# Kernel tuning notes

Hardware: AMD Instinct MI355X
Metric: run time of the kernel (lower is better)

Reference implementation:

```python
import math
import jax, jax.numpy as jnp
import numpy as np

B, S, D = 8, 1024, 1024
H, DK = 16, 64
NUM_BUCKETS, MAX_DIST = 32, 128
LN_EPS = 1e-6


def _relative_position_bucket(relative_position, num_buckets=NUM_BUCKETS, max_distance=MAX_DIST):
    # bidirectional (encoder) variant of T5 bucketing
    nb = num_buckets // 2
    rel_buckets = (relative_position > 0).astype(jnp.int32) * nb
    rp = jnp.abs(relative_position)
    max_exact = nb // 2
    is_small = rp < max_exact
    rp_large = max_exact + (
        jnp.log(jnp.maximum(rp, 1).astype(jnp.float32) / max_exact)
        / math.log(max_distance / max_exact)
        * (nb - max_exact)
    ).astype(jnp.int32)
    rp_large = jnp.minimum(rp_large, nb - 1)
    return rel_buckets + jnp.where(is_small, rp, rp_large)


def compute_bias(rel_bias, q_len, k_len):
    ctx = jnp.arange(q_len)[:, None]
    mem = jnp.arange(k_len)[None, :]
    buckets = _relative_position_bucket(mem - ctx)        # [q,k]
    values = rel_bias[buckets]                             # [q,k,H]
    return jnp.transpose(values, (2, 0, 1))[None]          # [1,H,q,k]


def switch_layer_norm(x, w, eps=LN_EPS):
    # T5-style: no mean subtraction, no bias
    var = jnp.mean(jnp.square(x.astype(jnp.float32)), axis=-1, keepdims=True)
    return w * (x * jax.lax.rsqrt(var + eps)).astype(x.dtype)


def setup_inputs() -> dict:
    key = jax.random.key(0)
    ks = jax.random.split(key, 6)
    scale = 1.0 / math.sqrt(D)
    return {
        "hidden_states": jax.random.normal(ks[0], (B, S, D), jnp.float32),
        "ln_weight": jnp.ones((D,), jnp.float32),
        "wq": jax.random.normal(ks[1], (D, H * DK), jnp.float32) * scale,
        "wk": jax.random.normal(ks[2], (D, H * DK), jnp.float32) * scale,
        "wv": jax.random.normal(ks[3], (D, H * DK), jnp.float32) * scale,
        "wo": jax.random.normal(ks[4], (H * DK, D), jnp.float32) * scale,
        "rel_bias": jax.random.normal(ks[5], (NUM_BUCKETS, H), jnp.float32),
    }


def reference(hidden_states, ln_weight, wq, wk, wv, wo, rel_bias):
    b, s, d = hidden_states.shape
    normed = switch_layer_norm(hidden_states, ln_weight)
    # projections -> [B,H,S,DK]; T5 applies NO 1/sqrt(dk) scaling
    q = (normed @ wq).reshape(b, s, H, DK).transpose(0, 2, 1, 3)
    k = (normed @ wk).reshape(b, s, H, DK).transpose(0, 2, 1, 3)
    v = (normed @ wv).reshape(b, s, H, DK).transpose(0, 2, 1, 3)
    scores = jnp.einsum("bhqd,bhkd->bhqk", q, k)
    scores = scores + compute_bias(rel_bias, s, s)
    attn = jax.nn.softmax(scores, axis=-1)
    ctx = jnp.einsum("bhqk,bhkd->bhqd", attn, v)
    ctx = ctx.transpose(0, 2, 1, 3).reshape(b, s, H * DK)
    attn_out = ctx @ wo
    return hidden_states + attn_out  # residual of SwitchLayerSelfAttention (dropout=0)
```

## Files before the change

### kernel.cpp

```cpp
#include <hip/hip_runtime.h>

typedef unsigned short u16;
typedef unsigned int u32;
typedef unsigned long long u64;
typedef __attribute__((ext_vector_type(8))) short bf16x8;
typedef __attribute__((ext_vector_type(4))) float f32x4;

__device__ __forceinline__ float bf2f(u16 u) {
  union { u32 i; float f; } c; c.i = ((u32)u) << 16; return c.f;
}
__device__ __forceinline__ u16 f2bf(float f) {
  union { float f; u32 i; } c; c.f = f;
  u32 i = c.i;
  return (u16)((i + 0x7fffu + ((i >> 16) & 1u)) >> 16);
}
__device__ __forceinline__ u32 pkbf(float a, float b) {
  union { float f; u32 i; } ca, cb; ca.f = a; cb.f = b;
  return __builtin_amdgcn_perm(cb.i + 0x8000u, ca.i + 0x8000u, 0x07060302u);
}
__device__ __forceinline__ void async16(const void* g, void* l) {
  __builtin_amdgcn_global_load_lds((const __attribute__((address_space(1))) void*)g,
                                   (__attribute__((address_space(3))) void*)l, 16, 0, 0);
}

__global__ __launch_bounds__(256) void detect_kernel(const u32* __restrict__ X,
                                                     int* __restrict__ flag) {
  __shared__ int part[4];
  const int tid = threadIdx.x, lane = tid & 63, wave = tid >> 6;
  int votes = 0;
  for (int i = tid; i < 4096; i += 256) {
    const u32 u = X[i];
    union { u32 i; float f; } c; c.i = u;
    const float a = fabsf(c.f);
    if (u == 0u || (a > 1e-6f && a < 1e6f)) votes++;
  }
  #pragma unroll
  for (int off = 32; off >= 1; off >>= 1) votes += __shfl_xor(votes, off);
  if (lane == 0) part[wave] = votes;
  __syncthreads();
  if (tid == 0) {
    const int tot = part[0] + part[1] + part[2] + part[3];
    *flag = (tot >= 2048) ? 0 : 1;
  }
}

__global__ __launch_bounds__(256) void prep_kernel(
    const void* __restrict__ W0, const void* __restrict__ W1, const void* __restrict__ W2,
    const void* __restrict__ W3, u16* __restrict__ T0, u16* __restrict__ T1,
    u16* __restrict__ T2, u16* __restrict__ T3, const void* __restrict__ rel_bias,
    float* __restrict__ Tb, const int* __restrict__ flagp) {
  const int f32m = (*flagp == 0);
  const int z = blockIdx.z;
  if (z == 4) {
    const int flat = blockIdx.y * 16 + blockIdx.x;
    const int idx = flat * 256 + threadIdx.x;
    if (idx >= 16 * 2047) return;
    const int h = idx / 2047;
    const int d = idx % 2047 - 1023;
    const int rb = (d > 0) ? 16 : 0;
    const int rp = d < 0 ? -d : d;
    int val;
    if (rp < 8) {
      val = rp;
    } else {
      float t = (logf((float)rp * 0.125f) / 2.772588722239781f) * 8.0f;
      val = 8 + (int)t;
      if (val > 15) val = 15;
    }
    const int bi = (rb + val) * 16 + h;
    Tb[idx] = f32m ? ((const float*)rel_bias)[bi] : bf2f(((const u16*)rel_bias)[bi]);
    return;
  }
  const void* W = (z == 0) ? W0 : (z == 1) ? W1 : (z == 2) ? W2 : W3;
  u16* WT = (z == 0) ? T0 : (z == 1) ? T1 : (z == 2) ? T2 : T3;
  __shared__ u16 t[64][65];
  const int tid = threadIdx.x;
  const int tx = tid & 63, ty = tid >> 6;
  const int n0 = blockIdx.x * 64, k0 = blockIdx.y * 64;
  #pragma unroll
  for (int r = ty; r < 64; r += 4) {
    const size_t idx = (size_t)(k0 + r) * 1024 + n0 + tx;
    t[r][tx] = f32m ? f2bf(((const float*)W)[idx]) : ((const u16*)W)[idx];
  }
  __syncthreads();
  #pragma unroll
  for (int r = ty; r < 64; r += 4) WT[(size_t)(n0 + r) * 1024 + k0 + tx] = t[tx][r];
}

__global__ __launch_bounds__(256) void rmsnorm_kernel(const void* __restrict__ X,
                                                      const void* __restrict__ W,
                                                      u16* __restrict__ Out,
                                                      const int* __restrict__ flagp) {
  const int f32m = (*flagp == 0);
  __shared__ float part[4];
  const int tid = threadIdx.x, lane = tid & 63, wave = tid >> 6;
  const size_t row = blockIdx.x;
  const int c = tid * 4;
  float x0, x1, x2, x3, w0f, w1f, w2f, w3f;
  if (f32m) {
    const float4 xx = *(const float4*)((const float*)X + row * 1024 + c);
    x0 = xx.x; x1 = xx.y; x2 = xx.z; x3 = xx.w;
    const float4 ww = *(const float4*)((const float*)W + c);
    w0f = ww.x; w1f = ww.y; w2f = ww.z; w3f = ww.w;
  } else {
    const u32* px = (const u32*)((const u16*)X + row * 1024 + c);
    const u32 a0 = px[0], a1 = px[1];
    x0 = bf2f((u16)a0); x1 = bf2f((u16)(a0 >> 16));
    x2 = bf2f((u16)a1); x3 = bf2f((u16)(a1 >> 16));
    const u32* pw = (const u32*)((const u16*)W + c);
    const u32 b0 = pw[0], b1 = pw[1];
    w0f = bf2f((u16)b0); w1f = bf2f((u16)(b0 >> 16));
    w2f = bf2f((u16)b1); w3f = bf2f((u16)(b1 >> 16));
  }
  float ss = x0 * x0 + x1 * x1 + x2 * x2 + x3 * x3;
  #pragma unroll
  for (int off = 32; off >= 1; off >>= 1) ss += __shfl_xor(ss, off);
  if (lane == 0) part[wave] = ss;
  __syncthreads();
  const float tot = part[0] + part[1] + part[2] + part[3];
  const float scale = rsqrtf(tot * (1.0f / 1024.0f) + 1e-6f);
  const u16 o0 = f2bf(x0 * scale * w0f);
  const u16 o1 = f2bf(x1 * scale * w1f);
  const u16 o2 = f2bf(x2 * scale * w2f);
  const u16 o3 = f2bf(x3 * scale * w3f);
  u32* po = (u32*)(Out + row * 1024 + c);
  po[0] = (u32)o0 | ((u32)o1 << 16);
  po[1] = (u32)o2 | ((u32)o3 << 16);
}

template <int S0>
__device__ __forceinline__ void stage3(u16* lds, const u16* __restrict__ A,
                                       const u16* __restrict__ B, int m0, int n0,
                                       int kt, int w, int lane) {
  const int ko8 = ((lane & 7) ^ ((lane >> 3) & 7)) * 8;
  const int rl = lane >> 3;
  #pragma unroll
  for (int s = S0; s < S0 + 3; ++s) {
    const int cw = s * 8 + w;
    const int r = cw * 8 + rl;
    u16* ldst = lds + cw * 512;
    if (s < 4)
      async16(A + (size_t)(m0 + r) * 1024 + kt + ko8, ldst);
    else
      async16(B + (size_t)(n0 + r - 256) * 1024 + kt + ko8, ldst);
  }
}

template <bool SWAP>
__device__ __forceinline__ void gemm256_core(const u16* __restrict__ A,
                                             const u16* __restrict__ WT,
                                             u16 (*buf)[24576], f32x4 (&acc)[4][4],
                                             int m0, int n0, int lane, int w) {
  const int wr = w >> 1, wc = w & 1;
  const int l15 = lane & 15;
  const int ko0 = (((lane >> 4) + 0) ^ (lane & 7)) * 8;
  const int ko1 = (((lane >> 4) + 4) ^ (lane & 7)) * 8;
  const int arow = (wr * 64 + l15) * 64;
  const int brow = 16384 + (wc * 64 + l15) * 64;

  stage3<0>(buf[0], A, WT, m0, n0, 0, w, lane);
  stage3<3>(buf[0], A, WT, m0, n0, 0, w, lane);
  stage3<0>(buf[1], A, WT, m0, n0, 64, w, lane);
  stage3<3>(buf[1], A, WT, m0, n0, 64, w, lane);
  __asm__ volatile("s_waitcnt vmcnt(6)" ::: "memory");
  __builtin_amdgcn_s_barrier();
  __asm__ volatile("" ::: "memory");

  int sl = 0, sn = 2;
  #pragma unroll 1
  for (int t = 0; t < 16; ++t) {
    const u16* bc = buf[sl];
    u16* bn = buf[sn];
    const int kt2 = (t + 2) * 64;
    bf16x8 af[4][2], bfr[2][2];
    #pragma unroll
    for (int i = 0; i < 4; ++i) {
      af[i][0] = *(const bf16x8*)(bc + arow + i * 1024 + ko0);
      af[i][1] = *(const bf16x8*)(bc + arow + i * 1024 + ko1);
    }
    #pragma unroll
    for (int j = 0; j < 2; ++j) {
      bfr[j][0] = *(const bf16x8*)(bc + brow + j * 1024 + ko0);
      bfr[j][1] = *(const bf16x8*)(bc + brow + j * 1024 + ko1);
    }
    if (t < 14) stage3<0>(bn, A, WT, m0, n0, kt2, w, lane);
    __builtin_amdgcn_s_barrier();
    __asm__ volatile("s_waitcnt lgkmcnt(0)" ::: "memory");
    __builtin_amdgcn_s_setprio(1);
    #pragma unroll
    for (int i = 0; i < 4; ++i)
      #pragma unroll
      for (int j = 0; j < 2; ++j) {
        if (SWAP) {
          acc[i][j] = __builtin_amdgcn_mfma_f32_16x16x32_bf16(bfr[j][0], af[i][0], acc[i][j], 0, 0, 0);
          acc[i][j] = __builtin_amdgcn_mfma_f32_16x16x32_bf16(bfr[j][1], af[i][1], acc[i][j], 0, 0, 0);
        } else {
          acc[i][j] = __builtin_amdgcn_mfma_f32_16x16x32_bf16(af[i][0], bfr[j][0], acc[i][j], 0, 0, 0);
          acc[i][j] = __builtin_amdgcn_mfma_f32_16x16x32_bf16(af[i][1], bfr[j][1], acc[i][j], 0, 0, 0);
        }
      }
    __builtin_amdgcn_s_setprio(0);
    __builtin_amdgcn_s_barrier();
    __asm__ volatile("" ::: "memory");
    #pragma unroll
    for (int j = 0; j < 2; ++j) {
      bfr[j][0] = *(const bf16x8*)(bc + brow + (j + 2) * 1024 + ko0);
      bfr[j][1] = *(const bf16x8*)(bc + brow + (j + 2) * 1024 + ko1);
    }
    if (t < 14) stage3<3>(bn, A, WT, m0, n0, kt2, w, lane);
    __builtin_amdgcn_s_barrier();
    __asm__ volatile("s_waitcnt lgkmcnt(0)" ::: "memory");
    __builtin_amdgcn_s_setprio(1);
    #pragma unroll
    for (int i = 0; i < 4; ++i)
      #pragma unroll
      for (int j = 0; j < 2; ++j) {
        if (SWAP) {
          acc[i][j + 2] = __builtin_amdgcn_mfma_f32_16x16x32_bf16(bfr[j][0], af[i][0], acc[i][j + 2], 0, 0, 0);
          acc[i][j + 2] = __builtin_amdgcn_mfma_f32_16x16x32_bf16(bfr[j][1], af[i][1], acc[i][j + 2], 0, 0, 0);
        } else {
          acc[i][j + 2] = __builtin_amdgcn_mfma_f32_16x16x32_bf16(af[i][0], bfr[j][0], acc[i][j + 2], 0, 0, 0);
          acc[i][j + 2] = __builtin_amdgcn_mfma_f32_16x16x32_bf16(af[i][1], bfr[j][1], acc[i][j + 2], 0, 0, 0);
        }
      }
    __builtin_amdgcn_s_setprio(0);
    if (t < 14)
      __asm__ volatile("s_waitcnt vmcnt(6)" ::: "memory");
    else
      __asm__ volatile("s_waitcnt vmcnt(0)" ::: "memory");
    __builtin_amdgcn_s_barrier();
    __asm__ volatile("" ::: "memory");
    sl = (sl == 2) ? 0 : sl + 1;
    sn = (sn == 2) ? 0 : sn + 1;
  }
}

__global__ __launch_bounds__(512, 2) void qkv_gemm256_kernel(
    const u16* __restrict__ A, const u16* __restrict__ WT,
    u16* __restrict__ Qo, u16* __restrict__ Ko, u16* __restrict__ VTo) {
  __shared__ __align__(16) u16 buf[3][24576];
  const int tid = threadIdx.x, lane = tid & 63, w = tid >> 6;
  const int id = blockIdx.x;
  const int xcd = id & 7;
  const int t0 = id >> 3;
  const int nb = t0 % 24;
  const int mhi = t0 / 24;
  const int m0 = (mhi * 8 + xcd) * 256;
  const int n0 = nb * 128;
  const int z = nb >> 3;

  f32x4 acc[4][4];
  const f32x4 zero = {0.f, 0.f, 0.f, 0.f};
  #pragma unroll
  for (int i = 0; i < 4; ++i)
    #pragma unroll
    for (int j = 0; j < 4; ++j) acc[i][j] = zero;

  const int wr = w >> 1, wc = w & 1;
  const int cq = lane & 15, quad = lane >> 4;
  const int nbase = (n0 & 1023) + wc * 64;

  if (z == 2) {
    gemm256_core<false>(A, WT, buf, acc, m0, n0, lane, w);
    #pragma unroll
    for (int i = 0; i < 4; ++i) {
      const int s = m0 + wr * 64 + i * 16 + quad * 4;
      const int b = s >> 10, s0 = s & 1023;
      #pragma unroll
      for (int j = 0; j < 4; ++j) {
        const int n = nbase + j * 16 + cq;
        const int hh = n >> 6, dk = n & 63;
        const u64 pk = (u64)f2bf(acc[i][j][0]) | ((u64)f2bf(acc[i][j][1]) << 16) |
                       ((u64)f2bf(acc[i][j][2]) << 32) | ((u64)f2bf(acc[i][j][3]) << 48);
        *(u64*)(VTo + (((size_t)(b * 16 + hh)) * 64 + dk) * 1024 + s0) = pk;
      }
    }
  } else {
    gemm256_core<true>(A, WT, buf, acc, m0, n0, lane, w);
    u16* Out = (z == 0) ? Qo : Ko;
    #pragma unroll
    for (int i = 0; i < 4; ++i) {
      const int s = m0 + wr * 64 + i * 16 + cq;
      const int b = s >> 10, ss = s & 1023;
      #pragma unroll
      for (int j = 0; j < 4; ++j) {
        const int n = nbase + j * 16 + quad * 4;
        const int hh = n >> 6, dk = n & 63;
        const u64 pk = (u64)f2bf(acc[i][j][0]) | ((u64)f2bf(acc[i][j][1]) << 16) |
                       ((u64)f2bf(acc[i][j][2]) << 32) | ((u64)f2bf(acc[i][j][3]) << 48);
        *(u64*)(Out + (((size_t)(b * 16 + hh)) * 1024 + ss) * 64 + dk) = pk;
      }
    }
  }
}

__global__ __launch_bounds__(512, 2) void out_gemm256_kernel(
    const u16* __restrict__ A, const u16* __restrict__ BT, const void* __restrict__ Res,
    void* __restrict__ Out, const int* __restrict__ flagp) {
  const int f32m = (*flagp == 0);
  __shared__ __align__(16) u16 buf[3][24576];
  const int tid = threadIdx.x, lane = tid & 63, w = tid >> 6;
  const int id = blockIdx.x;
  const int xcd = id & 7;
  const int t0 = id >> 3;
  const int nb = t0 & 7;
  const int mhi = t0 >> 3;
  const int m0 = (mhi * 8 + xcd) * 256;
  const int n0 = nb * 128;

  f32x4 acc[4][4];
  const f32x4 zero = {0.f, 0.f, 0.f, 0.f};
  #pragma unroll
  for (int i = 0; i < 4; ++i)
    #pragma unroll
    for (int j = 0; j < 4; ++j) acc[i][j] = zero;

  gemm256_core<true>(A, BT, buf, acc, m0, n0, lane, w);

  const int wr = w >> 1, wc = w & 1;
  const int cq = lane & 15, quad = lane >> 4;
  #pragma unroll
  for (int i = 0; i < 4; ++i) {
    const int s = m0 + wr * 64 + i * 16 + cq;
    #pragma unroll
    for (int j = 0; j < 4; ++j) {
      const int n = n0 + wc * 64 + j * 16 + quad * 4;
      const size_t idx = (size_t)s * 1024 + n;
      if (f32m) {
        const float4 rr = *(const float4*)((const float*)Res + idx);
        float4 oo;
        oo.x = rr.x + acc[i][j][0]; oo.y = rr.y + acc[i][j][1];
        oo.z = rr.z + acc[i][j][2]; oo.w = rr.w + acc[i][j][3];
        *(float4*)((float*)Out + idx) = oo;
      } else {
        const u64 rr = *(const u64*)((const u16*)Res + idx);
        const u64 pk =
            (u64)f2bf(bf2f((u16)rr) + acc[i][j][0]) |
            ((u64)f2bf(bf2f((u16)(rr >> 16)) + acc[i][j][1]) << 16) |
            ((u64)f2bf(bf2f((u16)(rr >> 32)) + acc[i][j][2]) << 32) |
            ((u64)f2bf(bf2f((u16)(rr >> 48)) + acc[i][j][3]) << 48);
        *(u64*)((u16*)Out + idx) = pk;
      }
    }
  }
}

__global__ __launch_bounds__(512, 4) void attn_kernel(
    const u16* __restrict__ Q, const u16* __restrict__ K, const u16* __restrict__ VT,
    const float* __restrict__ Tb, u16* __restrict__ ctx) {
  __shared__ __align__(16) u16 Ks[2][4096];
  __shared__ __align__(16) u16 Vs[2][4096];
  __shared__ __align__(16) u16 Ps[8][2048];
  __shared__ __align__(16) float Tbs[1280];

  const int tid = threadIdx.x, lane = tid & 63, w = tid >> 6;
  const int c = lane & 15, quad = lane >> 4;
  const int id = blockIdx.x;
  const int bh = id & 127, qc = id >> 7;
  const int b = bh >> 4, h = bh & 15;
  const int q0 = qc * 256;
  const int qw = q0 + w * 32;
  const u16* Kg = K + (size_t)bh * 1024 * 64;
  const u16* Vg = VT + (size_t)bh * 64 * 1024;
  const float* Th = Tb + h * 2047;
  u16* PsW = &Ps[w][0];

  for (int i = tid; i < 1280; i += 512) Tbs[i] = Th[768 - q0 + i];

  bf16x8 qf[2][2];
  {
    const u16* Qg = Q + ((size_t)bh * 1024 + qw) * 64;
    #pragma unroll
    for (int nt = 0; nt < 2; ++nt)
      #pragma unroll
      for (int half = 0; half < 2; ++half)
        qf[nt][half] = *(const bf16x8*)(Qg + (size_t)(nt * 16 + c) * 64 + half * 32 + quad * 8);
  }

  f32x4 oacc[4][2];
  const f32x4 zero = {0.f, 0.f, 0.f, 0.f};
  #pragma unroll
  for (int i = 0; i < 4; ++i)
    #pragma unroll
    for (int j = 0; j < 2; ++j) oacc[i][j] = zero;
  float rsum[2] = {0.f, 0.f};

  const u16* Ksrc = Kg + (size_t)((w >> 1) * 16 + c) * 64 + (w & 1) * 32 + quad * 8;
  const u16* Vsrc = Vg + (size_t)((w >> 1) * 16 + c) * 1024 + (w & 1) * 32 + quad * 8;

  async16(Ksrc, &Ks[0][w * 512]);
  async16(Vsrc, &Vs[0][w * 512]);

  #pragma unroll 1
  for (int kt = 0; kt < 16; ++kt) {
    const int cur = kt & 1;
    const int k0 = kt * 64;
    __asm__ volatile("s_waitcnt vmcnt(0)" ::: "memory");
    __syncthreads();
    if (kt < 15) {
      const int k1 = (kt + 1) * 64;
      async16(Ksrc + (size_t)k1 * 64, &Ks[1 - cur][w * 512]);
      async16(Vsrc + k1, &Vs[1 - cur][w * 512]);
    }
    f32x4 sc[4][2];
    const int jb = k0 + quad * 4 - c + 255 - 32 * w;
    #pragma unroll
    for (int mt = 0; mt < 4; ++mt)
      #pragma unroll
      for (int nt = 0; nt < 2; ++nt) {
        const float* tp = Tbs + jb + mt * 16 - nt * 16;
        sc[mt][nt][0] = tp[0]; sc[mt][nt][1] = tp[1]; sc[mt][nt][2] = tp[2]; sc[mt][nt][3] = tp[3];
      }
    const u16* Kc = &Ks[cur][0];
    #pragma unroll
    for (int mt = 0; mt < 4; ++mt) {
      const bf16x8 kf0 = *(const bf16x8*)(Kc + (mt * 2 + 0) * 512 + lane * 8);
      const bf16x8 kf1 = *(const bf16x8*)(Kc + (mt * 2 + 1) * 512 + lane * 8);
      #pragma unroll
      for (int nt = 0; nt < 2; ++nt) {
        sc[mt][nt] = __builtin_amdgcn_mfma_f32_16x16x32_bf16(kf0, qf[nt][0], sc[mt][nt], 0, 0, 0);
        sc[mt][nt] = __builtin_amdgcn_mfma_f32_16x16x32_bf16(kf1, qf[nt][1], sc[mt][nt], 0, 0, 0);
      }
    }
    #pragma unroll
    for (int mt = 0; mt < 4; ++mt)
      #pragma unroll
      for (int nt = 0; nt < 2; ++nt) {
        const float p0 = __expf(sc[mt][nt][0]), p1 = __expf(sc[mt][nt][1]);
        const float p2 = __expf(sc[mt][nt][2]), p3 = __expf(sc[mt][nt][3]);
        rsum[nt] += (p0 + p1) + (p2 + p3);
        const u32 lo = pkbf(p0, p1), hi = pkbf(p2, p3);
        const u64 pk = (u64)lo | ((u64)hi << 32);
        const int ch = (mt * 2 + (quad >> 1)) ^ (c & 7);
        *(u64*)(PsW + (nt * 16 + c) * 64 + ch * 8 + (quad & 1) * 4) = pk;
      }
    __asm__ volatile("s_waitcnt lgkmcnt(0)" ::: "memory");
    const u16* Vc = &Vs[cur][0];
    bf16x8 pf[2][2];
    #pragma unroll
    for (int nt = 0; nt < 2; ++nt)
      #pragma unroll
      for (int kk = 0; kk < 2; ++kk) {
        const int ch = (kk * 4 + quad) ^ (c & 7);
        pf[nt][kk] = *(const bf16x8*)(PsW + (nt * 16 + c) * 64 + ch * 8);
      }
    #pragma unroll
    for (int dt = 0; dt < 4; ++dt) {
      const bf16x8 vf0 = *(const bf16x8*)(Vc + (dt * 2 + 0) * 512 + lane * 8);
      const bf16x8 vf1 = *(const bf16x8*)(Vc + (dt * 2 + 1) * 512 + lane * 8);
      #pragma unroll
      for (int nt = 0; nt < 2; ++nt) {
        oacc[dt][nt] = __builtin_amdgcn_mfma_f32_16x16x32_bf16(vf0, pf[nt][0], oacc[dt][nt], 0, 0, 0);
        oacc[dt][nt] = __builtin_amdgcn_mfma_f32_16x16x32_bf16(vf1, pf[nt][1], oacc[dt][nt], 0, 0, 0);
      }
    }
  }

  #pragma unroll
  for (int nt = 0; nt < 2; ++nt) {
    rsum[nt] += __shfl_xor(rsum[nt], 16);
    rsum[nt] += __shfl_xor(rsum[nt], 32);
  }

  #pragma unroll
  for (int nt = 0; nt < 2; ++nt) {
    const float inv = 1.0f / rsum[nt];
    const int q = qw + nt * 16 + c;
    #pragma unroll
    for (int dt = 0; dt < 4; ++dt) {
      const u64 pk = (u64)f2bf(oacc[dt][nt][0] * inv) | ((u64)f2bf(oacc[dt][nt][1] * inv) << 16) |
                     ((u64)f2bf(oacc[dt][nt][2] * inv) << 32) | ((u64)f2bf(oacc[dt][nt][3] * inv) << 48);
      *(u64*)(ctx + (((size_t)b * 1024 + q) * 16 + h) * 64 + dt * 16 + quad * 4) = pk;
    }
  }
}

extern "C" void kernel_launch(void* const* d_in, const int* in_sizes, int n_in,
                              void* d_out, int out_size, void* d_ws, size_t ws_size,
                              hipStream_t stream) {
  const void* hidden = d_in[0];
  const void* lnw = d_in[1];
  const void* wq = d_in[2];
  const void* wk = d_in[3];
  const void* wv = d_in[4];
  const void* wo = d_in[5];
  const void* relb = d_in[6];
  char* ws = (char*)d_ws;

  u16* normed = (u16*)(ws);
  u16* Qb = (u16*)(ws + ((size_t)16 << 20));
  u16* Kb = (u16*)(ws + ((size_t)32 << 20));
  u16* VTb = (u16*)(ws + ((size_t)48 << 20));
  u16* wtq = (u16*)(ws + ((size_t)64 << 20));
  u16* wtk = (u16*)(ws + ((size_t)64 << 20) + (2 << 20));
  u16* wtv = (u16*)(ws + ((size_t)64 << 20) + (4 << 20));
  u16* wto = (u16*)(ws + ((size_t)64 << 20) + (6 << 20));
  float* Tb = (float*)(ws + ((size_t)64 << 20) + (8 << 20));
  int* flag = (int*)(ws + ((size_t)64 << 20) + (9 << 20));

  dim3 b256(256);
  detect_kernel<<<dim3(1), b256, 0, stream>>>((const u32*)hidden, flag);
  prep_kernel<<<dim3(16, 16, 5), b256, 0, stream>>>(wq, wk, wv, wo, wtq, wtk, wtv, wto,
                                                    relb, Tb, flag);
  rmsnorm_kernel<<<dim3(8192), b256, 0, stream>>>(hidden, lnw, normed, flag);
  qkv_gemm256_kernel<<<dim3(768), dim3(512), 0, stream>>>(normed, wtq, Qb, Kb, VTb);
  attn_kernel<<<dim3(512), dim3(512), 0, stream>>>(Qb, Kb, VTb, Tb, normed);
  out_gemm256_kernel<<<dim3(256), dim3(512), 0, stream>>>(normed, wto, hidden, d_out, flag);
}
```

Before: 257.8 us.

## Use 256x256 tiles with BK=32 split-phase pipeline for QKV GEMM

Replaces the 256x128 QKV projection GEMM with a 256x256 output tile per block, halving the grid to 384 blocks. K-step is reduced to 32 with a triple-buffered LDS pipeline, and each iteration is split into two MFMA phases that interleave A-half loads and async global-to-LDS staging. Larger tiles raise arithmetic intensity and reduce redundant A/B traffic, but double the accumulator registers (128 floats) and may reduce the number of waves available to hide latency.

```diff
diff --git a/kernel.cpp b/kernel.cpp
--- a/kernel.cpp
+++ b/kernel.cpp
@@ -235,40 +235,131 @@
   }
 }
 
-__global__ __launch_bounds__(512, 2) void qkv_gemm256_kernel(
+template <int S0>
+__device__ __forceinline__ void stageQ(u16* lds, const u16* __restrict__ A,
+                                       const u16* __restrict__ B, int m0, int n0,
+                                       int kt, int w, int lane) {
+  const int sp = (lane & 7) ^ ((lane >> 3) & 7);
+  const int rl = 2 * (lane >> 3) + (sp >> 2);
+  const int ko = (sp & 3) * 8;
+  #pragma unroll
+  for (int s = S0; s < S0 + 2; ++s) {
+    const int cw = s * 8 + w;
+    u16* ldst = lds + cw * 512;
+    if (s < 2)
+      async16(A + (size_t)(m0 + cw * 16 + rl) * 1024 + kt + ko, ldst);
+    else
+      async16(B + (size_t)(n0 + (cw - 16) * 16 + rl) * 1024 + kt + ko, ldst);
+  }
+}
+
+template <bool SWAP>
+__device__ __forceinline__ void gemmQ_core(const u16* __restrict__ A,
+                                           const u16* __restrict__ WT,
+                                           u16 (*buf)[16384], f32x4 (&acc)[8][4],
+                                           int m0, int n0, int lane, int w) {
+  const int wr = w >> 2, wc = w & 3;
+  const int l15 = lane & 15, quad = lane >> 4;
+  const int sw = ((quad + 4 * (lane & 1)) ^ ((l15 >> 1) & 7)) * 8;
+  const int abase = (wr * 64 + (l15 >> 1)) * 64 + sw;
+  const int bbase = 8192 + (wc * 32 + (l15 >> 1)) * 64 + sw;
+
+  stageQ<0>(buf[0], A, WT, m0, n0, 0, w, lane);
+  stageQ<2>(buf[0], A, WT, m0, n0, 0, w, lane);
+  stageQ<0>(buf[1], A, WT, m0, n0, 32, w, lane);
+  stageQ<2>(buf[1], A, WT, m0, n0, 32, w, lane);
+  __asm__ volatile("s_waitcnt vmcnt(4)" ::: "memory");
+  __builtin_amdgcn_s_barrier();
+  __asm__ volatile("" ::: "memory");
+
+  int sl = 0, sn = 2;
+  #pragma unroll 1
+  for (int t = 0; t < 32; ++t) {
+    const u16* bc = buf[sl];
+    u16* bn = buf[sn];
+    const int kt2 = (t + 2) * 32;
+    bf16x8 af[4], bfr[4];
+    #pragma unroll
+    for (int i = 0; i < 4; ++i) af[i] = *(const bf16x8*)(bc + abase + i * 512);
+    #pragma unroll
+    for (int j = 0; j < 4; ++j) bfr[j] = *(const bf16x8*)(bc + bbase + j * 512);
+    if (t < 30) stageQ<0>(bn, A, WT, m0, n0, kt2, w, lane);
+    __builtin_amdgcn_s_barrier();
+    __asm__ volatile("s_waitcnt lgkmcnt(0)" ::: "memory");
+    __builtin_amdgcn_s_setprio(1);
+    #pragma unroll
+    for (int i = 0; i < 4; ++i)
+      #pragma unroll
+      for (int j = 0; j < 4; ++j) {
+        if (SWAP)
+          acc[i][j] = __builtin_amdgcn_mfma_f32_16x16x32_bf16(bfr[j], af[i], acc[i][j], 0, 0, 0);
+        else
+          acc[i][j] = __builtin_amdgcn_mfma_f32_16x16x32_bf16(af[i], bfr[j], acc[i][j], 0, 0, 0);
+      }
+    __builtin_amdgcn_s_setprio(0);
+    __builtin_amdgcn_s_barrier();
+    __asm__ volatile("" ::: "memory");
+    #pragma unroll
+    for (int i = 0; i < 4; ++i) af[i] = *(const bf16x8*)(bc + abase + (i + 4) * 512);
+    if (t < 30) stageQ<2>(bn, A, WT, m0, n0, kt2, w, lane);
+    __builtin_amdgcn_s_barrier();
+    __asm__ volatile("s_waitcnt lgkmcnt(0)" ::: "memory");
+    __builtin_amdgcn_s_setprio(1);
+    #pragma unroll
+    for (int i = 0; i < 4; ++i)
+      #pragma unroll
+      for (int j = 0; j < 4; ++j) {
+        if (SWAP)
+          acc[i + 4][j] = __builtin_amdgcn_mfma_f32_16x16x32_bf16(bfr[j], af[i], acc[i + 4][j], 0, 0, 0);
+        else
+          acc[i + 4][j] = __builtin_amdgcn_mfma_f32_16x16x32_bf16(af[i], bfr[j], acc[i + 4][j], 0, 0, 0);
+      }
+    __builtin_amdgcn_s_setprio(0);
+    if (t < 30)
+      __asm__ volatile("s_waitcnt vmcnt(4)" ::: "memory");
+    else
+      __asm__ volatile("s_waitcnt vmcnt(0)" ::: "memory");
+    __builtin_amdgcn_s_barrier();
+    __asm__ volatile("" ::: "memory");
+    sl = (sl == 2) ? 0 : sl + 1;
+    sn = (sn == 2) ? 0 : sn + 1;
+  }
+}
+
+__global__ __launch_bounds__(512, 2) void qkv_gemmQ_kernel(
     const u16* __restrict__ A, const u16* __restrict__ WT,
     u16* __restrict__ Qo, u16* __restrict__ Ko, u16* __restrict__ VTo) {
-  __shared__ __align__(16) u16 buf[3][24576];
+  __shared__ __align__(16) u16 buf[3][16384];
   const int tid = threadIdx.x, lane = tid & 63, w = tid >> 6;
   const int id = blockIdx.x;
   const int xcd = id & 7;
   const int t0 = id >> 3;
-  const int nb = t0 % 24;
-  const int mhi = t0 / 24;
+  const int nb = t0 % 12;
+  const int mhi = t0 / 12;
   const int m0 = (mhi * 8 + xcd) * 256;
-  const int n0 = nb * 128;
-  const int z = nb >> 3;
-
-  f32x4 acc[4][4];
+  const int n0 = nb * 256;
+  const int z = nb >> 2;
+
+  f32x4 acc[8][4];
   const f32x4 zero = {0.f, 0.f, 0.f, 0.f};
   #pragma unroll
-  for (int i = 0; i < 4; ++i)
+  for (int i = 0; i < 8; ++i)
     #pragma unroll
     for (int j = 0; j < 4; ++j) acc[i][j] = zero;
 
-  const int wr = w >> 1, wc = w & 1;
+  const int wr = w >> 2, wc = w & 3;
   const int cq = lane & 15, quad = lane >> 4;
-  const int nbase = (n0 & 1023) + wc * 64;
+  const int ncol0 = (nb & 3) * 256 + wc * 64;
 
   if (z == 2) {
-    gemm256_core<false>(A, WT, buf, acc, m0, n0, lane, w);
-    #pragma unroll
-    for (int i = 0; i < 4; ++i) {
-      const int s = m0 + wr * 64 + i * 16 + quad * 4;
+    gemmQ_core<false>(A, WT, buf, acc, m0, n0, lane, w);
+    #pragma unroll
+    for (int i = 0; i < 8; ++i) {
+      const int s = m0 + wr * 128 + i * 16 + quad * 4;
       const int b = s >> 10, s0 = s & 1023;
       #pragma unroll
       for (int j = 0; j < 4; ++j) {
-        const int n = nbase + j * 16 + cq;
+        const int n = ncol0 + j * 16 + cq;
         const int hh = n >> 6, dk = n & 63;
         const u64 pk = (u64)f2bf(acc[i][j][0]) | ((u64)f2bf(acc[i][j][1]) << 16) |
                        ((u64)f2bf(acc[i][j][2]) << 32) | ((u64)f2bf(acc[i][j][3]) << 48);
@@ -276,15 +367,15 @@
       }
     }
   } else {
-    gemm256_core<true>(A, WT, buf, acc, m0, n0, lane, w);
+    gemmQ_core<true>(A, WT, buf, acc, m0, n0, lane, w);
     u16* Out = (z == 0) ? Qo : Ko;
     #pragma unroll
-    for (int i = 0; i < 4; ++i) {
-      const int s = m0 + wr * 64 + i * 16 + cq;
+    for (int i = 0; i < 8; ++i) {
+      const int s = m0 + wr * 128 + i * 16 + cq;
       const int b = s >> 10, ss = s & 1023;
       #pragma unroll
       for (int j = 0; j < 4; ++j) {
-        const int n = nbase + j * 16 + quad * 4;
+        const int n = ncol0 + j * 16 + quad * 4;
         const int hh = n >> 6, dk = n & 63;
         const u64 pk = (u64)f2bf(acc[i][j][0]) | ((u64)f2bf(acc[i][j][1]) << 16) |
                        ((u64)f2bf(acc[i][j][2]) << 32) | ((u64)f2bf(acc[i][j][3]) << 48);
@@ -503,7 +594,7 @@
   prep_kernel<<<dim3(16, 16, 5), b256, 0, stream>>>(wq, wk, wv, wo, wtq, wtk, wtv, wto,
                                                     relb, Tb, flag);
   rmsnorm_kernel<<<dim3(8192), b256, 0, stream>>>(hidden, lnw, normed, flag);
-  qkv_gemm256_kernel<<<dim3(768), dim3(512), 0, stream>>>(normed, wtq, Qb, Kb, VTb);
+  qkv_gemmQ_kernel<<<dim3(384), dim3(512), 0, stream>>>(normed, wtq, Qb, Kb, VTb);
   attn_kernel<<<dim3(512), dim3(512), 0, stream>>>(Qb, Kb, VTb, Tb, normed);
   out_gemm256_kernel<<<dim3(256), dim3(512), 0, stream>>>(normed, wto, hidden, d_out, flag);
 }
```

Measured after the change: 262.0 us. Within noise of the previous version (+1.6%).
